# Performance work log

Hardware: AMD Instinct MI355X
Metric: run time of the kernel (lower is better)

Reference implementation:

```python
import jax, jax.numpy as jnp
import numpy as np

B, T, N, H = 4096, 128, 128, 128  # batch, timesteps, input_size, encoder_num_hidden
EPS = 1e-5  # BatchNorm1d eps


def setup_inputs() -> dict:
    key = jax.random.key(0)
    ks = jax.random.split(key, 12)
    g = lambda k, shp, s=0.088: jax.random.normal(k, shp, dtype=jnp.float32) * s  # ~1/sqrt(H)
    return {
        "X": jax.random.normal(ks[0], (B, T, N), dtype=jnp.float32),
        "attn_w": g(ks[1], (2 * H + T,)),
        "attn_b": jnp.zeros((), jnp.float32),
        "bn_gamma": jnp.ones((N,), jnp.float32),
        "bn_beta": jnp.zeros((N,), jnp.float32),
        "W_ih0": g(ks[2], (4 * H, N)),
        "W_hh0": g(ks[3], (4 * H, H)),
        "b_ih0": g(ks[4], (4 * H,)),
        "b_hh0": g(ks[5], (4 * H,)),
        "W_ih1": g(ks[6], (4 * H, H)),
        "W_hh1": g(ks[7], (4 * H, H)),
        "b_ih1": g(ks[8], (4 * H,)),
        "b_hh1": g(ks[9], (4 * H,)),
    }


def _lstm_cell(x, h, c, W_ih, W_hh, b):
    # torch gate order: i, f, g, o
    gates = x @ W_ih.T + h @ W_hh.T + b  # (B, 4H)
    i, f, gg, o = jnp.split(gates, 4, axis=-1)
    c_new = jax.nn.sigmoid(f) * c + jax.nn.sigmoid(i) * jnp.tanh(gg)
    h_new = jax.nn.sigmoid(o) * jnp.tanh(c_new)
    return h_new, c_new


def reference(X, attn_w, attn_b, bn_gamma, bn_beta,
              W_ih0, W_hh0, b_ih0, b_hh0, W_ih1, W_hh1, b_ih1, b_hh1):
    # Attention input per step is cat(h_top repeat, s_top repeat, X^T) -> Linear(2H+T -> 1).
    # The X^T contribution is time-invariant; precompute it once.
    w_h, w_s, w_x = attn_w[:H], attn_w[H:2 * H], attn_w[2 * H:]
    Xp = jnp.transpose(X, (0, 2, 1))            # (B, N, T) driving-series view
    score_x = Xp @ w_x + attn_b                 # (B, N)
    b0 = b_ih0 + b_hh0
    b1 = b_ih1 + b_hh1

    def step(carry, x_t):
        h0, c0, h1, c1 = carry                  # layer0/layer1 hidden & cell (B, H)
        # h_n[-1], s_n[-1] are broadcast identically over all N features
        scores = score_x + (h1 @ w_h)[:, None] + (c1 @ w_s)[:, None]  # (B, N)
        alpha = jax.nn.softmax(scores, axis=1)
        x_tilde = alpha * x_t                   # (B, N)
        # BatchNorm1d in training mode: batch statistics over dim 0
        mean = jnp.mean(x_tilde, axis=0)
        var = jnp.var(x_tilde, axis=0)
        xb = (x_tilde - mean) * jax.lax.rsqrt(var + EPS) * bn_gamma + bn_beta
        # 2-layer LSTM single step (dropout inactive in eval)
        h0n, c0n = _lstm_cell(xb, h0, c0, W_ih0, W_hh0, b0)
        h1n, c1n = _lstm_cell(h0n, h1, c1, W_ih1, W_hh1, b1)
        return (h0n, c0n, h1n, c1n), (x_tilde, h1n)

    zeros = jnp.zeros((B, H), X.dtype)
    init = (zeros, zeros, zeros, zeros)
    Xt = jnp.transpose(X, (1, 0, 2))            # (T, B, N) for scan
    _, (xt_seq, he_seq) = jax.lax.scan(step, init, Xt)
    X_tilde = jnp.transpose(xt_seq, (1, 0, 2))   # (B, T, N)
    X_encoded = jnp.transpose(he_seq, (1, 0, 2)) # (B, T, H)
    return X_tilde, X_encoded
```

## Files before the change

### kernel.cpp

```cpp
#include <hip/hip_runtime.h>
#include <cstdint>
#include <cstddef>

#define B_ 4096
#define T_ 128
#define N_ 128
#define H_ 128
#define G4_ 512
#define KC_ 256
#define EPS_ 1e-5f

#define RPB_ 16
#define NB_ 256
#define W0K_ 128
#define W0P_ 136

typedef _Float16 f16x8 __attribute__((ext_vector_type(8)));
typedef _Float16 f16x4 __attribute__((ext_vector_type(4)));
typedef float f32x4 __attribute__((ext_vector_type(4)));

__device__ __forceinline__ float sigm_(float x) { return 1.f / (1.f + __expf(-x)); }
__device__ __forceinline__ float tanh_(float x) {
  float ax = fabsf(x);
  float e = __expf(-2.f * ax);
  float t = (1.f - e) / (1.f + e);
  return copysignf(t, x);
}

__global__ void k0_prep(const float* __restrict__ Wih0, const float* __restrict__ Whh0,
                        const float* __restrict__ bih0, const float* __restrict__ bhh0,
                        const float* __restrict__ Wih1, const float* __restrict__ Whh1,
                        const float* __restrict__ bih1, const float* __restrict__ bhh1,
                        _Float16* __restrict__ Wpack, float* __restrict__ bpack,
                        float* __restrict__ sumb, float* __restrict__ sqb) {
  int idx = blockIdx.x * blockDim.x + threadIdx.x;
  if (idx < 2 * G4_ * KC_) {
    int k = idx & (KC_ - 1);
    int j = (idx >> 8) & (G4_ - 1);
    int l = idx >> 17;
    const float* Wih = l ? Wih1 : Wih0;
    const float* Whh = l ? Whh1 : Whh0;
    float v = (k < N_) ? Wih[j * N_ + k] : Whh[j * N_ + (k - N_)];
    Wpack[idx] = (_Float16)v;
  }
  if (idx < 2 * G4_) {
    int j = idx & (G4_ - 1);
    bpack[idx] = (idx >> 9) ? (bih1[j] + bhh1[j]) : (bih0[j] + bhh0[j]);
  }
  if (idx < T_ * N_) { sumb[idx] = 0.f; sqb[idx] = 0.f; }
}

__global__ void k1_alpha(const float* __restrict__ X, const float* __restrict__ attn_w,
                         const float* __restrict__ attn_b, float* __restrict__ alpha) {
  __shared__ float wx[T_];
  __shared__ float red[4];
  int b = blockIdx.x;
  int n = threadIdx.x;
  wx[n] = attn_w[2 * H_ + n];
  __syncthreads();
  const float* xp = X + (size_t)b * T_ * N_ + n;
  float s = 0.f;
#pragma unroll 8
  for (int t = 0; t < T_; ++t) s = fmaf(xp[t * N_], wx[t], s);
  s += attn_b[0];
  float m = s;
#pragma unroll
  for (int off = 32; off >= 1; off >>= 1) m = fmaxf(m, __shfl_xor(m, off));
  if ((n & 63) == 0) red[n >> 6] = m;
  __syncthreads();
  m = fmaxf(red[0], red[1]);
  float e = __expf(s - m);
  float sm = e;
#pragma unroll
  for (int off = 32; off >= 1; off >>= 1) sm += __shfl_xor(sm, off);
  if ((n & 63) == 0) red[2 + (n >> 6)] = sm;
  __syncthreads();
  sm = red[2] + red[3];
  alpha[b * N_ + n] = e / sm;
}

__global__ void k2_xtilde(const float* __restrict__ X, const float* __restrict__ alpha,
                          float* __restrict__ out0, float* __restrict__ sumb,
                          float* __restrict__ sqb) {
  int t = blockIdx.x;
  int chunk = blockIdx.y;
  int n = threadIdx.x & (N_ - 1);
  int bi = threadIdx.x >> 7;
  float s = 0.f, q = 0.f;
  for (int it = 0; it < 128; ++it) {
    int b = (chunk << 8) + (it << 1) + bi;
    float a = alpha[b * N_ + n];
    size_t off = ((size_t)b * T_ + t) * N_ + n;
    float v = a * X[off];
    out0[off] = v;
    s += v;
    q += v * v;
  }
  __shared__ float ps[2][N_], pq[2][N_];
  ps[bi][n] = s;
  pq[bi][n] = q;
  __syncthreads();
  if (bi == 0) {
    atomicAdd(&sumb[t * N_ + n], ps[0][n] + ps[1][n]);
    atomicAdd(&sqb[t * N_ + n], pq[0][n] + pq[1][n]);
  }
}

__global__ void k3_finalize(const float* __restrict__ sumb, const float* __restrict__ sqb,
                            const float* __restrict__ gamma, const float* __restrict__ beta,
                            float* __restrict__ scale, float* __restrict__ shift) {
  int i = blockIdx.x * blockDim.x + threadIdx.x;
  if (i >= T_ * N_) return;
  int n = i & (N_ - 1);
  float mean = sumb[i] * (1.f / B_);
  float var = sqb[i] * (1.f / B_) - mean * mean;
  float rstd = rsqrtf(var + EPS_);
  float g = gamma[n];
  scale[i] = rstd * g;
  shift[i] = beta[n] - mean * rstd * g;
}

__global__ __launch_bounds__(512, 2) void k4_recur(
    const float* __restrict__ xt , const _Float16* __restrict__ Wpack,
    const float* __restrict__ bpack, const float* __restrict__ scale,
    const float* __restrict__ shift, float* __restrict__ out1) {
  __shared__ _Float16 W0l[G4_][W0P_];
  __shared__ _Float16 A0[RPB_][264];
  __shared__ _Float16 A1[RPB_][264];

  const int tid = threadIdx.x;
  const int w = tid >> 6;
  const int lane = tid & 63;
  const int quad = lane >> 4;
  const int l16 = lane & 15;
  const int nb = blockIdx.x;
  const int col = (w << 4) + l16;

  {
    const _Float16* src = Wpack + (size_t)tid * KC_;
#pragma unroll
    for (int kk = 0; kk < W0K_; kk += 8)
      *(f16x8*)&W0l[tid][kk] = *(const f16x8*)&src[kk];
  }

  f16x8 w1[4][8];
#pragma unroll
  for (int g = 0; g < 4; ++g) {
    const _Float16* src = Wpack + (size_t)(G4_ + (g << 7) + col) * KC_ + (quad << 3);
#pragma unroll
    for (int kb = 0; kb < 8; ++kb) w1[g][kb] = *(const f16x8*)&src[kb << 5];
  }

  float bia0[4], bia1[4];
#pragma unroll
  for (int g = 0; g < 4; ++g) {
    bia0[g] = bpack[(g << 7) + col];
    bia1[g] = bpack[G4_ + (g << 7) + col];
  }

  float c0[4], c1[4];
#pragma unroll
  for (int e = 0; e < 4; ++e) { c0[e] = 0.f; c1[e] = 0.f; }

  const int srow = tid >> 5;
  const int scol = (tid & 31) << 2;
  const size_t browbase = (size_t)(nb * RPB_ + srow) * T_;

  {
    f32x4 xv = *(const f32x4*)(xt + (browbase + 0) * N_ + scol);
    f32x4 sc = *(const f32x4*)(scale + scol);
    f32x4 sh = *(const f32x4*)(shift + scol);
    f16x4 hv;
#pragma unroll
    for (int e = 0; e < 4; ++e) hv[e] = (_Float16)fmaf(xv[e], sc[e], sh[e]);
    *(f16x4*)&A0[srow][scol] = hv;
    f16x4 z = {};
    *(f16x4*)&A0[srow][N_ + scol] = z;
    *(f16x4*)&A1[srow][N_ + scol] = z;
  }
  __syncthreads();

  for (int t = 0; t < T_; ++t) {
    f32x4 xn = {};
    if (t + 1 < T_) xn = *(const f32x4*)(xt + (browbase + t + 1) * N_ + scol);

    f32x4 acc[4] = {};
#pragma unroll
    for (int kb = 0; kb < 8; ++kb) {
      f16x8 a = *(const f16x8*)&A0[l16][(kb << 5) + (quad << 3)];
      if (kb < 4) {
#pragma unroll
        for (int g = 0; g < 4; ++g) {
          f16x8 bf = *(const f16x8*)&W0l[(g << 7) + col][(kb << 5) + (quad << 3)];
          acc[g] = __builtin_amdgcn_mfma_f32_16x16x32_f16(a, bf, acc[g], 0, 0, 0);
        }
      } else {
#pragma unroll
        for (int g = 0; g < 4; ++g) {
          f16x8 bf = *(const f16x8*)(Wpack + (size_t)((g << 7) + col) * KC_ +
                                     (kb << 5) + (quad << 3));
          acc[g] = __builtin_amdgcn_mfma_f32_16x16x32_f16(a, bf, acc[g], 0, 0, 0);
        }
      }
    }

    _Float16 h0h[4];
#pragma unroll
    for (int e = 0; e < 4; ++e) {
      float ig = acc[0][e] + bia0[0];
      float fg = acc[1][e] + bia0[1];
      float gg = acc[2][e] + bia0[2];
      float og = acc[3][e] + bia0[3];
      float cn = sigm_(fg) * c0[e] + sigm_(ig) * tanh_(gg);
      c0[e] = cn;
      h0h[e] = (_Float16)(sigm_(og) * tanh_(cn));
    }
    __syncthreads();
#pragma unroll
    for (int e = 0; e < 4; ++e) {
      A0[(quad << 2) + e][N_ + col] = h0h[e];
      A1[(quad << 2) + e][col] = h0h[e];
    }
    __syncthreads();

    f32x4 acc1[4] = {};
#pragma unroll
    for (int kb = 0; kb < 8; ++kb) {
      f16x8 a = *(const f16x8*)&A1[l16][(kb << 5) + (quad << 3)];
#pragma unroll
      for (int g = 0; g < 4; ++g)
        acc1[g] = __builtin_amdgcn_mfma_f32_16x16x32_f16(a, w1[g][kb], acc1[g], 0, 0, 0);
    }

    _Float16 h1h[4];
#pragma unroll
    for (int e = 0; e < 4; ++e) {
      float ig = acc1[0][e] + bia1[0];
      float fg = acc1[1][e] + bia1[1];
      float gg = acc1[2][e] + bia1[2];
      float og = acc1[3][e] + bia1[3];
      float cn = sigm_(fg) * c1[e] + sigm_(ig) * tanh_(gg);
      c1[e] = cn;
      float hn = sigm_(og) * tanh_(cn);
      h1h[e] = (_Float16)hn;
      out1[((size_t)(nb * RPB_ + (quad << 2) + e) * T_ + t) * H_ + col] = hn;
    }
    __syncthreads();
#pragma unroll
    for (int e = 0; e < 4; ++e)
      A1[(quad << 2) + e][N_ + col] = h1h[e];
    if (t + 1 < T_) {
      f32x4 sc = *(const f32x4*)(scale + (t + 1) * N_ + scol);
      f32x4 sh = *(const f32x4*)(shift + (t + 1) * N_ + scol);
      f16x4 hv;
#pragma unroll
      for (int e = 0; e < 4; ++e) hv[e] = (_Float16)fmaf(xn[e], sc[e], sh[e]);
      *(f16x4*)&A0[srow][scol] = hv;
    }
    __syncthreads();
  }
}

extern "C" void kernel_launch(void* const* d_in, const int* in_sizes, int n_in,
                              void* d_out, int out_size, void* d_ws, size_t ws_size,
                              hipStream_t stream) {
  const float* X = (const float*)d_in[0];
  const float* attnw = (const float*)d_in[1];
  const float* attnb = (const float*)d_in[2];
  const float* gamma = (const float*)d_in[3];
  const float* beta = (const float*)d_in[4];
  const float* Wih0 = (const float*)d_in[5];
  const float* Whh0 = (const float*)d_in[6];
  const float* bih0 = (const float*)d_in[7];
  const float* bhh0 = (const float*)d_in[8];
  const float* Wih1 = (const float*)d_in[9];
  const float* Whh1 = (const float*)d_in[10];
  const float* bih1 = (const float*)d_in[11];
  const float* bhh1 = (const float*)d_in[12];

  float* out0 = (float*)d_out;
  float* out1 = out0 + (size_t)B_ * T_ * N_;

  float* ws = (float*)d_ws;
  float* alpha = ws;
  float* sumb = alpha + (size_t)B_ * N_;
  float* sqb = sumb + T_ * N_;
  float* scale = sqb + T_ * N_;
  float* shift = scale + T_ * N_;
  float* bpack = shift + T_ * N_;
  _Float16* Wpack = (_Float16*)(bpack + 2 * G4_);

  k0_prep<<<1024, 256, 0, stream>>>(Wih0, Whh0, bih0, bhh0, Wih1, Whh1, bih1, bhh1,
                                    Wpack, bpack, sumb, sqb);
  k1_alpha<<<B_, 128, 0, stream>>>(X, attnw, attnb, alpha);
  k2_xtilde<<<dim3(T_, 16), 256, 0, stream>>>(X, alpha, out0, sumb, sqb);
  k3_finalize<<<64, 256, 0, stream>>>(sumb, sqb, gamma, beta, scale, shift);
  k4_recur<<<NB_, 512, 0, stream>>>(out0, Wpack, bpack, scale, shift, out1);
}
```

Before: 1.437 ms.

## Fuse attention softmax and x_tilde pass with per-block batchnorm partial sums

The separate alpha and x_tilde kernels become one kernel. Each block stages 8 batch rows of X in shared memory, computes the attention softmax, writes x_tilde, and accumulates per-(t,n) sum and sum-of-squares in registers. The per-block partials are written into the not-yet-written out1 region and reduced by a new kernel, which replaces the global atomics and avoids reading X twice. The layer-1 recurrence also preloads its A operands into registers before the MFMA loop. Risks are heavy register use (128 accumulators per thread) and 64KB of shared memory per block, which limits occupancy.

```diff
diff --git a/kernel.cpp b/kernel.cpp
--- a/kernel.cpp
+++ b/kernel.cpp
@@ -15,6 +15,10 @@
 #define W0K_ 128
 #define W0P_ 136
 
+#define KB_ 512
+#define ROWS_ 8
+#define PSBLK_ 16384
+
 typedef _Float16 f16x8 __attribute__((ext_vector_type(8)));
 typedef _Float16 f16x4 __attribute__((ext_vector_type(4)));
 typedef float f32x4 __attribute__((ext_vector_type(4)));
@@ -31,8 +35,7 @@
                         const float* __restrict__ bih0, const float* __restrict__ bhh0,
                         const float* __restrict__ Wih1, const float* __restrict__ Whh1,
                         const float* __restrict__ bih1, const float* __restrict__ bhh1,
-                        _Float16* __restrict__ Wpack, float* __restrict__ bpack,
-                        float* __restrict__ sumb, float* __restrict__ sqb) {
+                        _Float16* __restrict__ Wpack, float* __restrict__ bpack) {
   int idx = blockIdx.x * blockDim.x + threadIdx.x;
   if (idx < 2 * G4_ * KC_) {
     int k = idx & (KC_ - 1);
@@ -47,77 +50,96 @@
     int j = idx & (G4_ - 1);
     bpack[idx] = (idx >> 9) ? (bih1[j] + bhh1[j]) : (bih0[j] + bhh0[j]);
   }
-  if (idx < T_ * N_) { sumb[idx] = 0.f; sqb[idx] = 0.f; }
-}
-
-__global__ void k1_alpha(const float* __restrict__ X, const float* __restrict__ attn_w,
-                         const float* __restrict__ attn_b, float* __restrict__ alpha) {
+}
+
+__global__ __launch_bounds__(256, 2) void k12_fused(
+    const float* __restrict__ X, const float* __restrict__ attn_w,
+    const float* __restrict__ attn_b, float* __restrict__ out0,
+    float* __restrict__ psum, float* __restrict__ psq) {
+  __shared__ float xs[T_ * N_];
   __shared__ float wx[T_];
-  __shared__ float red[4];
-  int b = blockIdx.x;
-  int n = threadIdx.x;
-  wx[n] = attn_w[2 * H_ + n];
-  __syncthreads();
-  const float* xp = X + (size_t)b * T_ * N_ + n;
-  float s = 0.f;
+  __shared__ float redS[2][N_];
+  __shared__ float redM[4], redE[4];
+  const int tid = threadIdx.x;
+  const int blk = blockIdx.x;
+  const int n = tid & 127;
+  const int th = tid >> 7;
+  const int wv = tid >> 6;
+  if (tid < T_) wx[tid] = attn_w[2 * H_ + tid];
+  const float ab = attn_b[0];
+  float sum[64], sq[64];
+#pragma unroll
+  for (int i = 0; i < 64; ++i) { sum[i] = 0.f; sq[i] = 0.f; }
+
+  for (int rb = 0; rb < ROWS_; ++rb) {
+    const int b = blk * ROWS_ + rb;
+    const float* xb = X + (size_t)b * T_ * N_;
+    __syncthreads();
+#pragma unroll
+    for (int i = 0; i < 16; ++i) {
+      int fi = ((i << 8) + tid) << 2;
+      *(f32x4*)&xs[fi] = *(const f32x4*)&xb[fi];
+    }
+    __syncthreads();
+    float s = 0.f;
 #pragma unroll 8
-  for (int t = 0; t < T_; ++t) s = fmaf(xp[t * N_], wx[t], s);
-  s += attn_b[0];
-  float m = s;
-#pragma unroll
-  for (int off = 32; off >= 1; off >>= 1) m = fmaxf(m, __shfl_xor(m, off));
-  if ((n & 63) == 0) red[n >> 6] = m;
-  __syncthreads();
-  m = fmaxf(red[0], red[1]);
-  float e = __expf(s - m);
-  float sm = e;
-#pragma unroll
-  for (int off = 32; off >= 1; off >>= 1) sm += __shfl_xor(sm, off);
-  if ((n & 63) == 0) red[2 + (n >> 6)] = sm;
-  __syncthreads();
-  sm = red[2] + red[3];
-  alpha[b * N_ + n] = e / sm;
-}
-
-__global__ void k2_xtilde(const float* __restrict__ X, const float* __restrict__ alpha,
-                          float* __restrict__ out0, float* __restrict__ sumb,
-                          float* __restrict__ sqb) {
-  int t = blockIdx.x;
-  int chunk = blockIdx.y;
-  int n = threadIdx.x & (N_ - 1);
-  int bi = threadIdx.x >> 7;
+    for (int tt = 0; tt < 64; ++tt) {
+      int t = (th << 6) + tt;
+      s = fmaf(xs[t * N_ + n], wx[t], s);
+    }
+    redS[th][n] = s;
+    __syncthreads();
+    s = redS[0][n] + redS[1][n] + ab;
+    float m = s;
+#pragma unroll
+    for (int off = 32; off >= 1; off >>= 1) m = fmaxf(m, __shfl_xor(m, off));
+    if ((tid & 63) == 0) redM[wv] = m;
+    __syncthreads();
+    m = fmaxf(fmaxf(redM[0], redM[1]), fmaxf(redM[2], redM[3]));
+    float e = __expf(s - m);
+    float sm = e;
+#pragma unroll
+    for (int off = 32; off >= 1; off >>= 1) sm += __shfl_xor(sm, off);
+    if ((tid & 63) == 0) redE[wv] = sm;
+    __syncthreads();
+    sm = redE[0] + redE[1];
+    const float alpha = e / sm;
+    const size_t obase = ((size_t)b * T_ + (th << 6)) * N_ + n;
+#pragma unroll
+    for (int tt = 0; tt < 64; ++tt) {
+      float v = alpha * xs[((th << 6) + tt) * N_ + n];
+      sum[tt] += v;
+      sq[tt] += v * v;
+      out0[obase + (size_t)tt * N_] = v;
+    }
+  }
+  float* pbs = psum + (size_t)blk * PSBLK_ + th * 8192 + n;
+  float* pbq = psq + (size_t)blk * PSBLK_ + th * 8192 + n;
+#pragma unroll
+  for (int tt = 0; tt < 64; ++tt) {
+    pbs[tt * 128] = sum[tt];
+    pbq[tt * 128] = sq[tt];
+  }
+}
+
+__global__ void k3r(const float* __restrict__ psum, const float* __restrict__ psq,
+                    const float* __restrict__ gamma, const float* __restrict__ beta,
+                    float* __restrict__ scale, float* __restrict__ shift) {
+  const int t = blockIdx.x;
+  const int n = threadIdx.x;
+  const int th = t >> 6, tt = t & 63;
+  const size_t off = (size_t)th * 8192 + tt * 128 + n;
   float s = 0.f, q = 0.f;
-  for (int it = 0; it < 128; ++it) {
-    int b = (chunk << 8) + (it << 1) + bi;
-    float a = alpha[b * N_ + n];
-    size_t off = ((size_t)b * T_ + t) * N_ + n;
-    float v = a * X[off];
-    out0[off] = v;
-    s += v;
-    q += v * v;
-  }
-  __shared__ float ps[2][N_], pq[2][N_];
-  ps[bi][n] = s;
-  pq[bi][n] = q;
-  __syncthreads();
-  if (bi == 0) {
-    atomicAdd(&sumb[t * N_ + n], ps[0][n] + ps[1][n]);
-    atomicAdd(&sqb[t * N_ + n], pq[0][n] + pq[1][n]);
-  }
-}
-
-__global__ void k3_finalize(const float* __restrict__ sumb, const float* __restrict__ sqb,
-                            const float* __restrict__ gamma, const float* __restrict__ beta,
-                            float* __restrict__ scale, float* __restrict__ shift) {
-  int i = blockIdx.x * blockDim.x + threadIdx.x;
-  if (i >= T_ * N_) return;
-  int n = i & (N_ - 1);
-  float mean = sumb[i] * (1.f / B_);
-  float var = sqb[i] * (1.f / B_) - mean * mean;
+  for (int blk = 0; blk < KB_; ++blk) {
+    s += psum[(size_t)blk * PSBLK_ + off];
+    q += psq[(size_t)blk * PSBLK_ + off];
+  }
+  float mean = s * (1.f / B_);
+  float var = q * (1.f / B_) - mean * mean;
   float rstd = rsqrtf(var + EPS_);
   float g = gamma[n];
-  scale[i] = rstd * g;
-  shift[i] = beta[n] - mean * rstd * g;
+  scale[t * N_ + n] = rstd * g;
+  shift[t * N_ + n] = beta[n] - mean * rstd * g;
 }
 
 __global__ __launch_bounds__(512, 2) void k4_recur(
@@ -162,27 +184,27 @@
 #pragma unroll
   for (int e = 0; e < 4; ++e) { c0[e] = 0.f; c1[e] = 0.f; }
 
-  const int srow = tid >> 5;
-  const int scol = (tid & 31) << 2;
-  const size_t browbase = (size_t)(nb * RPB_ + srow) * T_;
+  const int sr = tid >> 5;
+  const int sc = (tid & 31) << 2;
+  const size_t browbase = (size_t)(nb * RPB_ + sr) * T_;
 
   {
-    f32x4 xv = *(const f32x4*)(xt + (browbase + 0) * N_ + scol);
-    f32x4 sc = *(const f32x4*)(scale + scol);
-    f32x4 sh = *(const f32x4*)(shift + scol);
+    f32x4 xv = *(const f32x4*)(xt + (browbase + 0) * N_ + sc);
+    f32x4 s4 = *(const f32x4*)(scale + sc);
+    f32x4 h4 = *(const f32x4*)(shift + sc);
     f16x4 hv;
 #pragma unroll
-    for (int e = 0; e < 4; ++e) hv[e] = (_Float16)fmaf(xv[e], sc[e], sh[e]);
-    *(f16x4*)&A0[srow][scol] = hv;
+    for (int e = 0; e < 4; ++e) hv[e] = (_Float16)fmaf(xv[e], s4[e], h4[e]);
+    *(f16x4*)&A0[sr][sc] = hv;
     f16x4 z = {};
-    *(f16x4*)&A0[srow][N_ + scol] = z;
-    *(f16x4*)&A1[srow][N_ + scol] = z;
+    *(f16x4*)&A0[sr][N_ + sc] = z;
+    *(f16x4*)&A1[sr][N_ + sc] = z;
   }
   __syncthreads();
 
   for (int t = 0; t < T_; ++t) {
     f32x4 xn = {};
-    if (t + 1 < T_) xn = *(const f32x4*)(xt + (browbase + t + 1) * N_ + scol);
+    if (t + 1 < T_) xn = *(const f32x4*)(xt + (browbase + t + 1) * N_ + sc);
 
     f32x4 acc[4] = {};
 #pragma unroll
@@ -223,13 +245,18 @@
     }
     __syncthreads();
 
+    f16x8 a1[8];
+#pragma unroll
+    for (int kb = 0; kb < 4; ++kb) {
+      a1[kb] = *(const f16x8*)&A1[l16][(kb << 5) + (quad << 3)];
+      a1[4 + kb] = *(const f16x8*)&A1[l16][128 + (kb << 5) + (quad << 3)];
+    }
     f32x4 acc1[4] = {};
 #pragma unroll
     for (int kb = 0; kb < 8; ++kb) {
-      f16x8 a = *(const f16x8*)&A1[l16][(kb << 5) + (quad << 3)];
 #pragma unroll
       for (int g = 0; g < 4; ++g)
-        acc1[g] = __builtin_amdgcn_mfma_f32_16x16x32_f16(a, w1[g][kb], acc1[g], 0, 0, 0);
+        acc1[g] = __builtin_amdgcn_mfma_f32_16x16x32_f16(a1[kb], w1[g][kb], acc1[g], 0, 0, 0);
     }
 
     _Float16 h1h[4];
@@ -250,12 +277,12 @@
     for (int e = 0; e < 4; ++e)
       A1[(quad << 2) + e][N_ + col] = h1h[e];
     if (t + 1 < T_) {
-      f32x4 sc = *(const f32x4*)(scale + (t + 1) * N_ + scol);
-      f32x4 sh = *(const f32x4*)(shift + (t + 1) * N_ + scol);
+      f32x4 s4 = *(const f32x4*)(scale + (t + 1) * N_ + sc);
+      f32x4 h4 = *(const f32x4*)(shift + (t + 1) * N_ + sc);
       f16x4 hv;
 #pragma unroll
-      for (int e = 0; e < 4; ++e) hv[e] = (_Float16)fmaf(xn[e], sc[e], sh[e]);
-      *(f16x4*)&A0[srow][scol] = hv;
+      for (int e = 0; e < 4; ++e) hv[e] = (_Float16)fmaf(xn[e], s4[e], h4[e]);
+      *(f16x4*)&A0[sr][sc] = hv;
     }
     __syncthreads();
   }
@@ -281,19 +308,18 @@
   float* out0 = (float*)d_out;
   float* out1 = out0 + (size_t)B_ * T_ * N_;
 
+  float* psum = out1;
+  float* psq = out1 + (size_t)KB_ * PSBLK_;
+
   float* ws = (float*)d_ws;
-  float* alpha = ws;
-  float* sumb = alpha + (size_t)B_ * N_;
-  float* sqb = sumb + T_ * N_;
-  float* scale = sqb + T_ * N_;
+  float* scale = ws;
   float* shift = scale + T_ * N_;
   float* bpack = shift + T_ * N_;
   _Float16* Wpack = (_Float16*)(bpack + 2 * G4_);
 
   k0_prep<<<1024, 256, 0, stream>>>(Wih0, Whh0, bih0, bhh0, Wih1, Whh1, bih1, bhh1,
-                                    Wpack, bpack, sumb, sqb);
-  k1_alpha<<<B_, 128, 0, stream>>>(X, attnw, attnb, alpha);
-  k2_xtilde<<<dim3(T_, 16), 256, 0, stream>>>(X, alpha, out0, sumb, sqb);
-  k3_finalize<<<64, 256, 0, stream>>>(sumb, sqb, gamma, beta, scale, shift);
+                                    Wpack, bpack);
+  k12_fused<<<KB_, 256, 0, stream>>>(X, attnw, attnb, out0, psum, psq);
+  k3r<<<T_, N_, 0, stream>>>(psum, psq, gamma, beta, scale, shift);
   k4_recur<<<NB_, 512, 0, stream>>>(out0, Wpack, bpack, scale, shift, out1);
 }
```

After: 1.385 ms. -3.6%, faster.
